# Optimization experiments

Measured on AMD Instinct MI355X. Metric: run time of the kernel, lower is better.

Reference implementation:

```python
import jax, jax.numpy as jnp
import numpy as np

SCALE = 2
GROUPS = 4


def _init_pos(scale, groups, dtype=jnp.float32):
    # h = arange((-s+1)/2, (s-1)/2 + 1) / s
    h = (jnp.arange(scale, dtype=dtype) - (scale - 1) / 2) / scale
    yy, xx = jnp.meshgrid(h, h, indexing='ij')
    pos = jnp.stack([xx, yy], axis=0)              # [2, s, s]
    # torch .repeat(1, groups, 1, 1) tiles along the size-2 dim -> [2*G, s, s]
    return jnp.tile(pos, (groups, 1, 1)).reshape(1, -1, 1, 1)  # [1, 2*G*s*s, 1, 1]


def _pixel_shuffle(x, r):
    B, C, H, W = x.shape
    Co = C // (r * r)
    x = x.reshape(B, Co, r, r, H, W)
    x = x.transpose(0, 1, 4, 2, 5, 3)              # [B, Co, H, r, W, r]
    return x.reshape(B, Co, H * r, W * r)


def _grid_sample_border(img, grid):
    # img: [N, C, H, W]; grid: [N, Ho, Wo, 2] in [-1, 1] (x, y); bilinear,
    # align_corners=False, padding_mode='border' (coords clamped first).
    N, C, H, W = img.shape
    gx, gy = grid[..., 0], grid[..., 1]
    ix = jnp.clip(((gx + 1) * W - 1) * 0.5, 0.0, W - 1)
    iy = jnp.clip(((gy + 1) * H - 1) * 0.5, 0.0, H - 1)
    x0f = jnp.floor(ix); y0f = jnp.floor(iy)
    wx = (ix - x0f)[:, None]                       # [N, 1, Ho, Wo]
    wy = (iy - y0f)[:, None]
    x0 = x0f.astype(jnp.int32); y0 = y0f.astype(jnp.int32)
    x1 = jnp.minimum(x0 + 1, W - 1); y1 = jnp.minimum(y0 + 1, H - 1)

    def gather(im, y, x):                          # im [C,H,W], y/x [Ho,Wo]
        return im[:, y, x]                         # [C, Ho, Wo]
    gv = jax.vmap(gather)

    return ((1 - wy) * ((1 - wx) * gv(img, y0, x0) + wx * gv(img, y0, x1))
            + wy * ((1 - wx) * gv(img, y1, x0) + wx * gv(img, y1, x1)))


def setup_inputs() -> dict:
    key = jax.random.key(0)
    k1, k2 = jax.random.split(key)
    B, C, H, W = 16, 64, 128, 128
    out_ch = 2 * GROUPS * SCALE ** 2               # 32
    x = jax.random.normal(k1, (B, C, H, W), dtype=jnp.float32)
    w_off = jax.random.normal(k2, (out_ch, C), dtype=jnp.float32) * 0.001
    b_off = jnp.zeros((out_ch,), dtype=jnp.float32)
    return {"x": x, "w_off": w_off, "b_off": b_off}


def reference(x, w_off, b_off):
    B, C, H, W = x.shape
    s, G = SCALE, GROUPS
    # 1x1 conv offset, scaled by 0.25, plus fixed sub-pixel init positions
    offset = jnp.einsum('bchw,oc->bohw', x, w_off) + b_off[None, :, None, None]
    offset = offset * 0.25 + _init_pos(s, G, x.dtype)   # [B, 2*G*s*s, H, W]

    off = offset.reshape(B, 2, G * s * s, H, W)
    cx = jnp.arange(W, dtype=x.dtype) + 0.5
    cy = jnp.arange(H, dtype=x.dtype) + 0.5
    yy, xx = jnp.meshgrid(cy, cx, indexing='ij')
    coords = jnp.stack([xx, yy], axis=0)[None, :, None]  # [1, 2, 1, H, W]
    norm = jnp.array([W, H], dtype=x.dtype).reshape(1, 2, 1, 1, 1)
    coords = 2 * (coords + off) / norm - 1               # [B, 2, G*s*s, H, W]

    coords = _pixel_shuffle(coords.reshape(B, 2 * G * s * s, H, W), s)  # [B, 2G, sH, sW]
    grid = coords.reshape(B, 2, G, s * H, s * W)
    grid = grid.transpose(0, 2, 3, 4, 1).reshape(B * G, s * H, s * W, 2)

    out = _grid_sample_border(x.reshape(B * G, C // G, H, W), grid)
    return out.reshape(B, C, s * H, s * W)
```

## Files before the change

### kernel.cpp

```cpp
#include <hip/hip_runtime.h>


namespace {
constexpr int BB = 16;
constexpr int CC = 64;
constexpr int HH = 128;
constexpr int WW = 128;
constexpr int HW = HH * WW;
constexpr int OW = 2 * WW;
constexpr int OHW = 4 * HW;
constexpr int TH = 8, TW = 32;
constexpr int TILES = (HH / TH) * (WW / TW);
}

__global__ __launch_bounds__(256, 4)
void dysample_kernel(const float* __restrict__ x,
                     const float* __restrict__ w_off,
                     const float* __restrict__ b_off,
                     float* __restrict__ out) {
    __shared__ float2 coords[16][256];

    const int tid  = threadIdx.x;
    const int b    = blockIdx.x >> 6;
    const int tile = blockIdx.x & 63;
    const int th0  = (tile >> 2) * TH;
    const int tw0  = (tile & 3) * TW;
    const int ty   = tid >> 5;
    const int tx   = tid & 31;
    const int h    = th0 + ty;
    const int w    = tw0 + tx;

    float acc[32];
#pragma unroll
    for (int o = 0; o < 32; ++o) acc[o] = b_off[o];

    const float* xb = x + b * (CC * HW) + h * WW + w;
#pragma unroll
    for (int half = 0; half < 2; ++half) {
        float xv[32];
#pragma unroll
        for (int c = 0; c < 32; ++c) xv[c] = xb[(half * 32 + c) * HW];
#pragma unroll
        for (int o = 0; o < 32; ++o) {
            float a = acc[o];
#pragma unroll
            for (int c = 0; c < 32; ++c)
                a = fmaf(xv[c], w_off[o * 64 + half * 32 + c], a);
            acc[o] = a;
        }
    }

    const float fw = (float)w, fh = (float)h;
#pragma unroll
    for (int q = 0; q < 16; ++q) {
        const int g = q >> 2, r1 = (q >> 1) & 1, r2 = q & 1;
        const float init = (((g & 1) ? r1 : r2) ? 0.25f : -0.25f);
        const float offx = fmaf(acc[q],      0.25f, init);
        const float offy = fmaf(acc[q + 16], 0.25f, init);
        float ix = ((fw + 0.5f) + offx) - 0.5f;
        float iy = ((fh + 0.5f) + offy) - 0.5f;
        ix = fminf(fmaxf(ix, 0.0f), (float)(WW - 1));
        iy = fminf(fmaxf(iy, 0.0f), (float)(HH - 1));
        coords[q][tid] = make_float2(ix, iy);
    }
    __syncthreads();

    for (int g = 0; g < 4; ++g) {
        const float* xg = x + (b * CC + g * 16) * HW;
        float* og = out + (size_t)(b * CC + g * 16) * OHW;
#pragma unroll
        for (int rep = 0; rep < 4; ++rep) {
            const int p  = rep * 256 + tid;
            const int oy = p >> 6;
            const int ox = p & 63;
            const int q   = (g << 2) | ((oy & 1) << 1) | (ox & 1);
            const int pix = ((oy >> 1) << 5) | (ox >> 1);
            const float2 cc = coords[q][pix];
            const float x0f = floorf(cc.x), y0f = floorf(cc.y);
            const float wx = cc.x - x0f, wy = cc.y - y0f;
            const int x0 = (int)x0f, y0 = (int)y0f;
            const int x1 = min(x0 + 1, WW - 1);
            const int y1 = min(y0 + 1, HH - 1);
            const int o00 = y0 * WW + x0;
            const int o01 = y0 * WW + x1;
            const int o10 = y1 * WW + x0;
            const int o11 = y1 * WW + x1;
            const int oidx = (th0 * 2 + oy) * OW + (tw0 * 2 + ox);
#pragma unroll
            for (int c = 0; c < 16; ++c) {
                const float* xs = xg + c * HW;
                const float v00 = xs[o00], v01 = xs[o01];
                const float v10 = xs[o10], v11 = xs[o11];
                const float top = fmaf(wx, v01 - v00, v00);
                const float bot = fmaf(wx, v11 - v10, v10);
                og[c * OHW + oidx] = fmaf(wy, bot - top, top);
            }
        }
    }
}

extern "C" void kernel_launch(void* const* d_in, const int* in_sizes, int n_in,
                              void* d_out, int out_size, void* d_ws, size_t ws_size,
                              hipStream_t stream) {
    const float* x     = (const float*)d_in[0];
    const float* w_off = (const float*)d_in[1];
    const float* b_off = (const float*)d_in[2];
    float* out = (float*)d_out;
    (void)in_sizes; (void)n_in; (void)out_size; (void)d_ws; (void)ws_size;
    dysample_kernel<<<dim3(BB * TILES), dim3(256), 0, stream>>>(x, w_off, b_off, out);
}
```

Baseline: 431.0 us.

## Split groups across two blocks, store fp16 offsets, write paired float2 outputs nontemporally

```diff
diff --git a/kernel.cpp b/kernel.cpp
--- a/kernel.cpp
+++ b/kernel.cpp
@@ -1,8 +1,8 @@
 #include <hip/hip_runtime.h>
+#include <hip/hip_fp16.h>
 
 
 namespace {
-constexpr int BB = 16;
 constexpr int CC = 64;
 constexpr int HH = 128;
 constexpr int WW = 128;
@@ -10,90 +10,118 @@
 constexpr int OW = 2 * WW;
 constexpr int OHW = 4 * HW;
 constexpr int TH = 8, TW = 32;
-constexpr int TILES = (HH / TH) * (WW / TW);
+typedef float vfloat2 __attribute__((ext_vector_type(2)));
 }
 
-__global__ __launch_bounds__(256, 4)
+__global__ __launch_bounds__(256, 8)
 void dysample_kernel(const float* __restrict__ x,
                      const float* __restrict__ w_off,
                      const float* __restrict__ b_off,
                      float* __restrict__ out) {
-    __shared__ float2 coords[16][256];
+    __shared__ __half2 offh[8][256];
 
-    const int tid  = threadIdx.x;
-    const int b    = blockIdx.x >> 6;
-    const int tile = blockIdx.x & 63;
+    const int tid = threadIdx.x;
+    const int gg   = blockIdx.x & 1;
+    const int tile = (blockIdx.x >> 1) & 63;
+    const int b    = blockIdx.x >> 7;
     const int th0  = (tile >> 2) * TH;
     const int tw0  = (tile & 3) * TW;
     const int ty   = tid >> 5;
     const int tx   = tid & 31;
     const int h    = th0 + ty;
     const int w    = tw0 + tx;
+    const int q0   = gg * 8;
 
-    float acc[32];
+    float accx[8], accy[8];
 #pragma unroll
-    for (int o = 0; o < 32; ++o) acc[o] = b_off[o];
+    for (int j = 0; j < 8; ++j) {
+        accx[j] = b_off[q0 + j];
+        accy[j] = b_off[q0 + j + 16];
+    }
 
     const float* xb = x + b * (CC * HW) + h * WW + w;
 #pragma unroll
-    for (int half = 0; half < 2; ++half) {
-        float xv[32];
+    for (int chunk = 0; chunk < 4; ++chunk) {
+        float xv[16];
 #pragma unroll
-        for (int c = 0; c < 32; ++c) xv[c] = xb[(half * 32 + c) * HW];
+        for (int c = 0; c < 16; ++c) xv[c] = xb[(chunk * 16 + c) * HW];
 #pragma unroll
-        for (int o = 0; o < 32; ++o) {
-            float a = acc[o];
+        for (int j = 0; j < 8; ++j) {
+            float ax = accx[j], ay = accy[j];
+            const float* wx_ = w_off + (q0 + j) * 64 + chunk * 16;
+            const float* wy_ = wx_ + 16 * 64;
 #pragma unroll
-            for (int c = 0; c < 32; ++c)
-                a = fmaf(xv[c], w_off[o * 64 + half * 32 + c], a);
-            acc[o] = a;
+            for (int c = 0; c < 16; ++c) ax = fmaf(xv[c], wx_[c], ax);
+#pragma unroll
+            for (int c = 0; c < 16; ++c) ay = fmaf(xv[c], wy_[c], ay);
+            accx[j] = ax; accy[j] = ay;
         }
     }
 
-    const float fw = (float)w, fh = (float)h;
 #pragma unroll
-    for (int q = 0; q < 16; ++q) {
-        const int g = q >> 2, r1 = (q >> 1) & 1, r2 = q & 1;
+    for (int j = 0; j < 8; ++j) {
+        const int q = q0 + j, g = q >> 2, r1 = (q >> 1) & 1, r2 = q & 1;
         const float init = (((g & 1) ? r1 : r2) ? 0.25f : -0.25f);
-        const float offx = fmaf(acc[q],      0.25f, init);
-        const float offy = fmaf(acc[q + 16], 0.25f, init);
-        float ix = ((fw + 0.5f) + offx) - 0.5f;
-        float iy = ((fh + 0.5f) + offy) - 0.5f;
-        ix = fminf(fmaxf(ix, 0.0f), (float)(WW - 1));
-        iy = fminf(fmaxf(iy, 0.0f), (float)(HH - 1));
-        coords[q][tid] = make_float2(ix, iy);
+        const float offx = fmaf(accx[j], 0.25f, init);
+        const float offy = fmaf(accy[j], 0.25f, init);
+        offh[j][tid] = __floats2half2_rn(offx, offy);
     }
     __syncthreads();
 
-    for (int g = 0; g < 4; ++g) {
+    const int k   = tid & 31;
+    const float fw = (float)(tw0 + k);
+#pragma unroll
+    for (int gi = 0; gi < 2; ++gi) {
+        const int g = gg * 2 + gi;
         const float* xg = x + (b * CC + g * 16) * HW;
         float* og = out + (size_t)(b * CC + g * 16) * OHW;
 #pragma unroll
-        for (int rep = 0; rep < 4; ++rep) {
-            const int p  = rep * 256 + tid;
-            const int oy = p >> 6;
-            const int ox = p & 63;
-            const int q   = (g << 2) | ((oy & 1) << 1) | (ox & 1);
-            const int pix = ((oy >> 1) << 5) | (ox >> 1);
-            const float2 cc = coords[q][pix];
-            const float x0f = floorf(cc.x), y0f = floorf(cc.y);
-            const float wx = cc.x - x0f, wy = cc.y - y0f;
-            const int x0 = (int)x0f, y0 = (int)y0f;
-            const int x1 = min(x0 + 1, WW - 1);
-            const int y1 = min(y0 + 1, HH - 1);
-            const int o00 = y0 * WW + x0;
-            const int o01 = y0 * WW + x1;
-            const int o10 = y1 * WW + x0;
-            const int o11 = y1 * WW + x1;
-            const int oidx = (th0 * 2 + oy) * OW + (tw0 * 2 + ox);
+        for (int rep = 0; rep < 2; ++rep) {
+            const int oy  = rep * 8 + (ty);
+            const int jq  = gi * 4 + ((oy & 1) << 1);
+            const int pix = ((oy >> 1) << 5) | k;
+            const float2 o0 = __half22float2(offh[jq][pix]);
+            const float2 o1 = __half22float2(offh[jq + 1][pix]);
+            const float fh = (float)(th0 + (oy >> 1));
+
+            float ix0 = ((fw + 0.5f) + o0.x) - 0.5f;
+            float iy0 = ((fh + 0.5f) + o0.y) - 0.5f;
+            float ix1 = ((fw + 0.5f) + o1.x) - 0.5f;
+            float iy1 = ((fh + 0.5f) + o1.y) - 0.5f;
+            ix0 = fminf(fmaxf(ix0, 0.0f), 127.0f);
+            iy0 = fminf(fmaxf(iy0, 0.0f), 127.0f);
+            ix1 = fminf(fmaxf(ix1, 0.0f), 127.0f);
+            iy1 = fminf(fmaxf(iy1, 0.0f), 127.0f);
+
+            const float x0f0 = floorf(ix0), y0f0 = floorf(iy0);
+            const float x0f1 = floorf(ix1), y0f1 = floorf(iy1);
+            const float wx0 = ix0 - x0f0, wy0 = iy0 - y0f0;
+            const float wx1 = ix1 - x0f1, wy1 = iy1 - y0f1;
+            const int xa0 = (int)x0f0, ya0 = (int)y0f0;
+            const int xa1 = (int)x0f1, ya1 = (int)y0f1;
+            const int xb0 = min(xa0 + 1, WW - 1), yb0 = min(ya0 + 1, HH - 1);
+            const int xb1 = min(xa1 + 1, WW - 1), yb1 = min(ya1 + 1, HH - 1);
+            const int a00 = ya0 * WW + xa0, a01 = ya0 * WW + xb0;
+            const int a10 = yb0 * WW + xa0, a11 = yb0 * WW + xb0;
+            const int b00 = ya1 * WW + xa1, b01 = ya1 * WW + xb1;
+            const int b10 = yb1 * WW + xa1, b11 = yb1 * WW + xb1;
+            const int oidx = (th0 * 2 + oy) * OW + (tw0 * 2 + 2 * k);
+
 #pragma unroll
             for (int c = 0; c < 16; ++c) {
                 const float* xs = xg + c * HW;
-                const float v00 = xs[o00], v01 = xs[o01];
-                const float v10 = xs[o10], v11 = xs[o11];
-                const float top = fmaf(wx, v01 - v00, v00);
-                const float bot = fmaf(wx, v11 - v10, v10);
-                og[c * OHW + oidx] = fmaf(wy, bot - top, top);
+                const float va00 = xs[a00], va01 = xs[a01];
+                const float va10 = xs[a10], va11 = xs[a11];
+                const float vb00 = xs[b00], vb01 = xs[b01];
+                const float vb10 = xs[b10], vb11 = xs[b11];
+                const float t0 = fmaf(wx0, va01 - va00, va00);
+                const float u0 = fmaf(wx0, va11 - va10, va10);
+                const float t1 = fmaf(wx1, vb01 - vb00, vb00);
+                const float u1 = fmaf(wx1, vb11 - vb10, vb10);
+                vfloat2 r;
+                r.x = fmaf(wy0, u0 - t0, t0);
+                r.y = fmaf(wy1, u1 - t1, t1);
+                __builtin_nontemporal_store(r, (vfloat2*)(og + c * OHW + oidx));
             }
         }
     }
@@ -107,5 +135,5 @@
     const float* b_off = (const float*)d_in[2];
     float* out = (float*)d_out;
     (void)in_sizes; (void)n_in; (void)out_size; (void)d_ws; (void)ws_size;
-    dysample_kernel<<<dim3(BB * TILES), dim3(256), 0, stream>>>(x, w_off, b_off, out);
+    dysample_kernel<<<dim3(16 * 64 * 2), dim3(256), 0, stream>>>(x, w_off, b_off, out);
 }
```

After: 382.8 us. -11.2%, faster.
